# Kernel tuning notes

Hardware: AMD Instinct MI355X
Metric: run time of the kernel (lower is better)

The kernel has to match this reference:

```python
import jax, jax.numpy as jnp
import numpy as np

TEMP = 0.7
TOPK_RATIO = 0.75
BN_EPS = 1e-5  # eval-mode BN with running_mean=0, running_var=1


def conv3x3(x, w):
    # x: [N,C,H,W], w: [O,I,3,3], stride 1, pad 1
    return jax.lax.conv_general_dilated(x, w, (1, 1), 'SAME',
                                        dimension_numbers=('NCHW', 'OIHW', 'NCHW'))


def bn(x, g, b):
    scale = g / jnp.sqrt(1.0 + BN_EPS)
    return x * scale[:, None, None] + b[:, None, None]


def glu(x):
    c = x.shape[1] // 2
    return x[:, :c] * jax.nn.sigmoid(x[:, c:])


def resblock(x, w1, g1, b1, w2, g2, b2):
    out = glu(bn(conv3x3(x, w1), g1, b1))
    out = bn(conv3x3(out, w2), g2, b2)
    return out + x


def refined_attention(h_code, word_embs, w_ctx, mask):
    B, C, H, W = h_code.shape
    Q = H * W
    S = word_embs.shape[2]
    # conv_context is a 1x1 conv (no bias): pure channel projection
    sourceT = jnp.einsum('oc,bcs->bos', w_ctx, word_embs)   # [B, idf, S]
    target = h_code.reshape(B, C, Q)                        # [B, idf, Q]
    attn = jnp.einsum('bcq,bcs->bqs', target, sourceT)      # [B, Q, S]
    attn = attn.reshape(B * Q, S) / TEMP
    # faithful to torch: mask.repeat(queryL, 1) tiles mask over rows
    mask_exp = jnp.tile(mask, (Q, 1))                       # [B*Q, S]
    attn = jnp.where(mask_exp, -jnp.inf, attn)
    if TOPK_RATIO < 1.0 and S > 1:
        k = max(1, int(S * TOPK_RATIO))
        topk_vals, _ = jax.lax.top_k(attn, k)               # sorted desc
        threshold = topk_vals[:, -1:]                       # min of top-k
        attn = jnp.where(attn < threshold, -jnp.inf, attn)
    p = jax.nn.softmax(attn, axis=1)
    nan_rows = jnp.any(jnp.isnan(p), axis=1, keepdims=True)
    p = jnp.where(nan_rows, 1.0 / S, p)                     # uniform fallback
    p = p.reshape(B, Q, S)
    attn_t = jnp.swapaxes(p, 1, 2)                          # [B, S, Q]
    wctx = jnp.einsum('bos,bsq->boq', sourceT, attn_t).reshape(B, C, H, W)
    att_map = attn_t.reshape(B, S, H, W)
    return wctx, att_map


def upsample2x(x):
    return jnp.repeat(jnp.repeat(x, 2, axis=2), 2, axis=3)


def reference(h_code, c_code, word_embs, w_ctx,
              r0_w1, r0_g1, r0_b1, r0_w2, r0_g2, r0_b2,
              r1_w1, r1_g1, r1_b1, r1_w2, r1_g2, r1_b2,
              up_w, up_g, up_b, mask):
    # c_code is in the signature of NEXT_STAGE_G.forward but unused (as in AttnGAN)
    c_code_att, att = refined_attention(h_code, word_embs, w_ctx, mask)
    h_c = jnp.concatenate([h_code, c_code_att], axis=1)     # [B, 2*ngf, H, W]
    out = resblock(h_c, r0_w1, r0_g1, r0_b1, r0_w2, r0_g2, r0_b2)
    out = resblock(out, r1_w1, r1_g1, r1_b1, r1_w2, r1_g2, r1_b2)
    # upBlock: nearest upsample x2 -> conv3x3(2ngf, 2ngf) -> BN -> GLU -> ngf
    out = glu(bn(conv3x3(upsample2x(out), up_w), up_g, up_b))
    return out, att


def setup_inputs() -> dict:
    key = jax.random.key(0)
    ks = jax.random.split(key, 24)
    B, ngf, H, W = 8, 64, 128, 128
    nef, ncf, S = 256, 100, 32
    C2 = 2 * ngf  # 128
    std = 0.02
    inp = {
        'h_code': jax.random.normal(ks[0], (B, ngf, H, W), jnp.float32),
        'c_code': jax.random.normal(ks[1], (B, ncf), jnp.float32),
        'word_embs': jax.random.normal(ks[2], (B, nef, S), jnp.float32),
        'mask': jax.random.randint(ks[3], (B, S), 0, 2).astype(bool),
        'w_ctx': jax.random.normal(ks[4], (ngf, nef), jnp.float32) * std,
    }
    for i, base in enumerate([5, 11]):
        inp[f'r{i}_w1'] = jax.random.normal(ks[base + 0], (2 * C2, C2, 3, 3), jnp.float32) * std
        inp[f'r{i}_g1'] = jnp.ones((2 * C2,), jnp.float32)
        inp[f'r{i}_b1'] = jnp.zeros((2 * C2,), jnp.float32)
        inp[f'r{i}_w2'] = jax.random.normal(ks[base + 3], (C2, C2, 3, 3), jnp.float32) * std
        inp[f'r{i}_g2'] = jnp.ones((C2,), jnp.float32)
        inp[f'r{i}_b2'] = jnp.zeros((C2,), jnp.float32)
    inp['up_w'] = jax.random.normal(ks[17], (2 * ngf, C2, 3, 3), jnp.float32) * std
    inp['up_g'] = jnp.ones((2 * ngf,), jnp.float32)
    inp['up_b'] = jnp.zeros((2 * ngf,), jnp.float32)
    return inp
```

## Files before the change

### kernel.cpp

```cpp
#include <hip/hip_runtime.h>
#include <math.h>


#define B_N 8
#define NGF 64
#define HC 128
#define WC 128
#define QN (HC*WC)
#define NEF 256
#define SN 32
#define TEMP_INV (1.0f/0.7f)
#define BN_SC 0.99999500003749969f
#define TOPK 24

typedef _Float16 f16;
typedef __attribute__((ext_vector_type(8))) _Float16 f16x8;
typedef __attribute__((ext_vector_type(4))) _Float16 f16x4;
typedef __attribute__((ext_vector_type(4))) float f32x4;

__device__ __forceinline__ void gload16(const void* g, void* l) {
    __builtin_amdgcn_global_load_lds(
        (const __attribute__((address_space(1))) void*)g,
        (__attribute__((address_space(3))) void*)l,
        16, 0, 0);
}

__global__ void prep_mask_k(const void* __restrict__ mraw,
                            unsigned* __restrict__ mbits,
                            unsigned* __restrict__ zp) {
    __shared__ int mode;
    if (threadIdx.x == 0) {
        const unsigned* u = (const unsigned*)mraw;
        bool i32 = true, f32m = true;
        for (int i = 0; i < 64; ++i) {
            unsigned v = u[i];
            if (v > 1u) i32 = false;
            if (v != 0u && v != 0x3F800000u) f32m = false;
        }
        mode = i32 ? 0 : (f32m ? 1 : 2);
    }
    __syncthreads();
    int t = threadIdx.x;
    if (t < 64) zp[(t >> 4) * 262144 + (t & 15)] = 0u;
    if (t < B_N) {
        unsigned bits = 0;
        for (int s = 0; s < SN; ++s) {
            int idx = t * SN + s;
            bool on;
            if (mode == 0)      on = ((const int*)mraw)[idx] != 0;
            else if (mode == 1) on = ((const float*)mraw)[idx] != 0.0f;
            else                on = ((const unsigned char*)mraw)[idx] != 0;
            if (on) bits |= (1u << s);
        }
        mbits[t] = bits;
    }
}

__global__ __launch_bounds__(256) void source_t_k(
        const float* __restrict__ w_ctx, const float* __restrict__ word_embs,
        float* __restrict__ sT) {
    int b = blockIdx.x >> 3;
    int o = ((blockIdx.x & 7) << 3) + (threadIdx.x >> 5);
    int s = threadIdx.x & 31;
    const float* wrow = w_ctx + (size_t)o * NEF;
    const float* wb = word_embs + (size_t)b * NEF * SN + s;
    float acc = 0.0f;
    #pragma unroll 8
    for (int c = 0; c < NEF; ++c) acc += wrow[c] * wb[(size_t)c * SN];
    sT[((size_t)b * NGF + o) * SN + s] = acc;
}

__global__ __launch_bounds__(256) void attention_k(
        const float* __restrict__ h_code, const float* __restrict__ sT,
        const unsigned* __restrict__ mbits,
        float* __restrict__ att_out,
        f16* __restrict__ hc) {
    int r0 = blockIdx.x * 256;
    int b = r0 >> 14;
    __shared__ float st[NGF * SN];
    const float* stg = sT + (size_t)b * NGF * SN;
    for (int i = threadIdx.x; i < NGF * SN; i += 256) st[i] = stg[i];
    __syncthreads();
    int q = (r0 & (QN - 1)) + threadIdx.x;

    const float* hb = h_code + (size_t)b * NGF * QN + q;
    f16* hcb = hc + (size_t)b * QN * 128;

    float a[SN];
    #pragma unroll
    for (int s = 0; s < SN; ++s) a[s] = 0.0f;
    for (int g8 = 0; g8 < 8; ++g8) {
        f16x8 t;
        #pragma unroll
        for (int r = 0; r < 8; ++r) {
            float v = hb[(size_t)(g8 * 8 + r) * QN];
            t[r] = (f16)v;
            #pragma unroll
            for (int s = 0; s < SN; ++s) a[s] += v * st[(g8 * 8 + r) * SN + s];
        }
        *(f16x8*)(hcb + ((size_t)g8 * QN + q) * 8) = t;
    }
    unsigned mb = mbits[q & 7];
    #pragma unroll
    for (int s = 0; s < SN; ++s)
        a[s] = ((mb >> s) & 1u) ? -INFINITY : a[s] * TEMP_INV;

    float thr = -INFINITY;
    #pragma unroll
    for (int s = 0; s < SN; ++s) {
        int rank = 0;
        #pragma unroll
        for (int j = 0; j < SN; ++j)
            rank += (a[j] > a[s]) || (a[j] == a[s] && j < s);
        if (rank == TOPK - 1) thr = a[s];
    }
    float m = -INFINITY;
    #pragma unroll
    for (int s = 0; s < SN; ++s) {
        if (a[s] < thr) a[s] = -INFINITY;
        m = fmaxf(m, a[s]);
    }
    float p[SN];
    if (m == -INFINITY) {
        #pragma unroll
        for (int s = 0; s < SN; ++s) p[s] = 1.0f / SN;
    } else {
        float sum = 0.0f;
        #pragma unroll
        for (int s = 0; s < SN; ++s) { p[s] = __expf(a[s] - m); sum += p[s]; }
        float inv = 1.0f / sum;
        #pragma unroll
        for (int s = 0; s < SN; ++s) p[s] *= inv;
    }
    float* ao = att_out + (size_t)b * SN * QN + q;
    #pragma unroll
    for (int s = 0; s < SN; ++s) ao[(size_t)s * QN] = p[s];
    for (int g8 = 0; g8 < 8; ++g8) {
        f16x8 t;
        #pragma unroll
        for (int r = 0; r < 8; ++r) {
            float acc = 0.0f;
            #pragma unroll
            for (int s = 0; s < SN; ++s) acc += st[(g8 * 8 + r) * SN + s] * p[s];
            t[r] = (f16)acc;
        }
        *(f16x8*)(hcb + ((size_t)(8 + g8) * QN + q) * 8) = t;
    }
}

__global__ __launch_bounds__(256) void wt_transform_k(
        const float* __restrict__ w, f16* __restrict__ wt,
        int total, int HALF ) {
    int idx = blockIdx.x * 256 + threadIdx.x;
    if (idx >= total) return;
    int e   = idx & 7;
    int gp  = (idx >> 3) & 3;
    int cop = (idx >> 5) & 63;
    int u   = idx >> 11;
    int t   = u % 9;
    int v   = u / 9;
    int cc  = v & 3;
    int cb  = v >> 2;
    int g   = gp ^ ((cop >> 1) & 3);
    int ci  = cc * 32 + g * 8 + e;
    int co  = HALF ? (cop < 32 ? cb * 32 + cop : HALF + cb * 32 + (cop - 32))
                   : cb * 64 + cop;
    wt[idx] = (f16)w[((size_t)co * 128 + ci) * 9 + t];
}

__global__ __launch_bounds__(256) void wt_up_transform_k(
        const float* __restrict__ w, f16* __restrict__ wt) {
    int idx = blockIdx.x * 256 + threadIdx.x;
    int e   = idx & 7;
    int gp  = (idx >> 3) & 3;
    int cop = (idx >> 5) & 63;
    int tap = (idx >> 11) & 3;
    int pw  = (idx >> 13) & 1;
    int cc  = (idx >> 14) & 3;
    int ph  = (idx >> 16) & 1;
    int cb  = (idx >> 17) & 1;
    int g   = gp ^ ((cop >> 1) & 3);
    int ci  = cc * 32 + g * 8 + e;
    int co  = cop < 32 ? cb * 32 + cop : 64 + cb * 32 + (cop - 32);
    int ra = tap >> 1, bb = tap & 1;
    const float* wp = w + ((size_t)co * 128 + ci) * 9;
    float acc = 0.0f;
    #pragma unroll
    for (int kh = 0; kh < 3; ++kh) {
        int rma = (ph == 0) ? (kh == 0 ? 0 : 1) : (kh == 2 ? 1 : 0);
        if (rma != ra) continue;
        #pragma unroll
        for (int kw = 0; kw < 3; ++kw) {
            int cma = (pw == 0) ? (kw == 0 ? 0 : 1) : (kw == 2 ? 1 : 0);
            if (cma == bb) acc += wp[kh * 3 + kw];
        }
    }
    wt[idx] = (f16)acc;
}

template<int COUT, bool GLU, bool RES, bool UP, int HOUT, int WOUT, bool FINAL>
__global__ __launch_bounds__(256) void conv_mfma_k(
        const f16* __restrict__ in, const f16* __restrict__ wt,
        const float* __restrict__ gamma, const float* __restrict__ beta,
        const f16* __restrict__ res, f16* __restrict__ outh,
        float* __restrict__ outf, const char* __restrict__ zeros) {
    constexpr int HALF = COUT / 2;
    constexpr int OCH  = GLU ? HALF : COUT;
    constexpr int HIN  = UP ? HOUT / 2 : HOUT;
    constexpr int WIN  = UP ? WOUT / 2 : WOUT;
    constexpr int RPT  = 256 / WOUT;
    constexpr int ROWS_IN = UP ? 2 : RPT + 2;
    constexpr int NIN_G   = ROWS_IN * 520;
    constexpr int NIN_IT  = (NIN_G + 255) / 256;
    constexpr int NIN_PAD = NIN_IT * 256;
    constexpr int NTAP    = UP ? 4 : 9;
    constexpr int WBYTES  = UP ? 32768 : 36864;
    constexpr int WIT     = WBYTES / 4096;

    __shared__ char smem[NIN_PAD * 16 + WBYTES];
    char* sW = smem + NIN_PAD * 16;

    const int tid = threadIdx.x, lane = tid & 63, wv = tid >> 6;
    const int l15 = lane & 15, kg = lane >> 4;
    const int b = blockIdx.z, cb = blockIdx.y, qt = blockIdx.x;
    const int q0 = qt * 256;
    const int h0 = q0 / WOUT;
    const int ph = UP ? (h0 & 1) : 0;
    const int p  = wv >> 1;
    const int jq = ((wv & 1) << 6) + l15;

    f32x4 acc[4][4];
    #pragma unroll
    for (int m = 0; m < 4; ++m)
        #pragma unroll
        for (int n = 0; n < 4; ++n) acc[m][n] = (f32x4){0.f, 0.f, 0.f, 0.f};

    const f16* inb = in + (size_t)b * HIN * WIN * 128;
    const char* wtb = UP
        ? (const char*)wt + (size_t)(cb * 2 + ph) * 131072
        : (const char*)wt + (size_t)cb * 147456;

    const char* srcK[NIN_IT];
    #pragma unroll
    for (int k = 0; k < NIN_IT; ++k) {
        int idx = (k << 8) + tid;
        int r = idx / 520;
        int rem = idx - r * 520;
        int wi = rem >> 2, gp = rem & 3;
        int g = gp ^ ((wi >> 1) & 3);
        const char* s = zeros;
        if (UP) {
            int sh = (h0 >> 1) + r - 1 + ph;
            int sw = wi - 1;
            if (r < 2 && (unsigned)sh < (unsigned)HIN && (unsigned)sw < (unsigned)WIN)
                s = (const char*)(inb + (((size_t)g * (HIN * WIN) + (size_t)sh * WIN + sw) << 3));
        } else {
            int gh = h0 - 1 + r;
            int gw = wi - 1;
            if (r < ROWS_IN && (unsigned)gh < (unsigned)HOUT && (unsigned)gw < (unsigned)WOUT)
                s = (const char*)(inb + (((size_t)g * (HIN * WIN) + (size_t)gh * WIN + gw) << 3));
        }
        srcK[k] = s;
    }
    const int dstB = (tid & 192) << 4;

    for (int cc = 0; cc < 4; ++cc) {
        #pragma unroll
        for (int k = 0; k < NIN_IT; ++k)
            gload16(srcK[k] + (cc << 20), smem + (k << 12) + dstB);
        const char* wsrc = wtb + cc * WBYTES + (tid << 4);
        #pragma unroll
        for (int k = 0; k < WIT; ++k)
            gload16(wsrc + (k << 12), sW + (k << 12) + dstB);
        __syncthreads();

        #pragma unroll
        for (int t = 0; t < NTAP; ++t) {
            f16x8 af[4], bf[4];
            const int tapbase = UP ? ((p * 4 + t) << 12) : (t << 12);
            #pragma unroll
            for (int m = 0; m < 4; ++m) {
                int co = m * 16 + l15;
                af[m] = *(const f16x8*)(sW + tapbase + (co << 6)
                                        + ((kg ^ ((co >> 1) & 3)) << 4));
            }
            #pragma unroll
            for (int n = 0; n < 4; ++n) {
                int off;
                if (UP) {
                    int si = jq + (n << 4) + (t & 1) + p;
                    off = (t >> 1) * 8320 + si * 64 + ((kg ^ ((si >> 1) & 3)) << 4);
                } else {
                    const int kh = t / 3, kw = t % 3;
                    int row = (wv >> 1) + kh;
                    int wi = ((wv & 1) << 6) + (n << 4) + l15 + kw;
                    off = row * 8320 + wi * 64 + ((kg ^ ((wi >> 1) & 3)) << 4);
                }
                bf[n] = *(const f16x8*)(smem + off);
            }
            #pragma unroll
            for (int m = 0; m < 4; ++m)
                #pragma unroll
                for (int n = 0; n < 4; ++n)
                    acc[m][n] = __builtin_amdgcn_mfma_f32_16x16x32_f16(af[m], bf[n], acc[m][n], 0, 0, 0);
        }
        __syncthreads();
    }

    const int r4 = kg * 4;
    if (GLU) {
        #pragma unroll
        for (int mv = 0; mv < 2; ++mv) {
            const int v0 = cb * 32 + mv * 16 + r4;
            float s1[4], o1[4], s2[4], o2[4];
            #pragma unroll
            for (int r = 0; r < 4; ++r) {
                s1[r] = gamma[v0 + r] * BN_SC;        o1[r] = beta[v0 + r];
                s2[r] = gamma[v0 + r + HALF] * BN_SC; o2[r] = beta[v0 + r + HALF];
            }
            #pragma unroll
            for (int n = 0; n < 4; ++n) {
                float ov[4];
                #pragma unroll
                for (int r = 0; r < 4; ++r) {
                    float yv = acc[mv][n][r] * s1[r] + o1[r];
                    float zv = acc[mv + 2][n][r] * s2[r] + o2[r];
                    ov[r] = yv / (1.0f + __expf(-zv));
                }
                if (FINAL) {
                    const int w = UP ? 2 * (jq + (n << 4)) + p
                                     : ((wv << 6) + (n << 4) + l15) % WOUT;
                    const int h = UP ? h0 : h0 + ((wv << 6) + (n << 4) + l15) / WOUT;
                    #pragma unroll
                    for (int r = 0; r < 4; ++r)
                        outf[(((size_t)b * OCH + v0 + r) * HOUT + h) * WOUT + w] = ov[r];
                } else {
                    const int qc = (wv << 6) + (n << 4) + l15;
                    f16x4 tv;
                    #pragma unroll
                    for (int r = 0; r < 4; ++r) tv[r] = (f16)ov[r];
                    *(f16x4*)(outh + ((((size_t)b * (OCH / 8) + (v0 >> 3)) << 14)
                                      + q0 + qc) * 8 + (v0 & 7)) = tv;
                }
            }
        }
    } else {
        #pragma unroll
        for (int m = 0; m < 4; ++m) {
            const int c0 = cb * 64 + m * 16 + r4;
            float s[4], o[4];
            #pragma unroll
            for (int r = 0; r < 4; ++r) {
                s[r] = gamma[c0 + r] * BN_SC; o[r] = beta[c0 + r];
            }
            #pragma unroll
            for (int n = 0; n < 4; ++n) {
                const int qc = (wv << 6) + (n << 4) + l15;
                const size_t gaddr = ((((size_t)b * 16 + (c0 >> 3)) << 14) + q0 + qc) * 8 + (c0 & 7);
                float ov[4];
                #pragma unroll
                for (int r = 0; r < 4; ++r) ov[r] = acc[m][n][r] * s[r] + o[r];
                if (RES) {
                    f16x4 rv = *(const f16x4*)(res + gaddr);
                    #pragma unroll
                    for (int r = 0; r < 4; ++r) ov[r] += (float)rv[r];
                }
                f16x4 tv;
                #pragma unroll
                for (int r = 0; r < 4; ++r) tv[r] = (f16)ov[r];
                *(f16x4*)(outh + gaddr) = tv;
            }
        }
    }
}

extern "C" void kernel_launch(void* const* d_in, const int* in_sizes, int n_in,
                              void* d_out, int out_size, void* d_ws, size_t ws_size,
                              hipStream_t stream) {
    (void)in_sizes; (void)n_in; (void)out_size; (void)ws_size;
    const float* h_code    = (const float*)d_in[0];
    const float* word_embs = (const float*)d_in[2];
    const void*  mask      = d_in[3];
    const float* w_ctx     = (const float*)d_in[4];
    const float* r0_w1 = (const float*)d_in[5];
    const float* r0_g1 = (const float*)d_in[6];
    const float* r0_b1 = (const float*)d_in[7];
    const float* r0_w2 = (const float*)d_in[8];
    const float* r0_g2 = (const float*)d_in[9];
    const float* r0_b2 = (const float*)d_in[10];
    const float* r1_w1 = (const float*)d_in[11];
    const float* r1_g1 = (const float*)d_in[12];
    const float* r1_b1 = (const float*)d_in[13];
    const float* r1_w2 = (const float*)d_in[14];
    const float* r1_g2 = (const float*)d_in[15];
    const float* r1_b2 = (const float*)d_in[16];
    const float* up_w  = (const float*)d_in[17];
    const float* up_g  = (const float*)d_in[18];
    const float* up_b  = (const float*)d_in[19];

    float* outp = (float*)d_out;
    float* attp = outp + (size_t)B_N * NGF * 4 * HC * WC;

    unsigned* mbits = (unsigned*)d_ws;
    float* sT  = (float*)((char*)d_ws + 1024);
    char* zeros = (char*)d_ws + ((size_t)4 << 20);
    f16* hcA   = (f16*)((char*)d_ws + ((size_t)8 << 20));
    f16* wtbuf = (f16*)((char*)d_ws + ((size_t)40 << 20));

    const int W1_TOT = 4 * 4 * 9 * 64 * 32;
    const int W2_TOT = 2 * 4 * 9 * 64 * 32;
    const int WUP_TOT = 2 * 2 * 4 * 2 * 4 * 64 * 32;
    f16* Wr0c1 = wtbuf;
    f16* Wr0c2 = Wr0c1 + W1_TOT;
    f16* Wr1c1 = Wr0c2 + W2_TOT;
    f16* Wr1c2 = Wr1c1 + W1_TOT;
    f16* Wup   = Wr1c2 + W2_TOT;

    f16* Bbuf = (f16*)d_out;
    f16* Cbuf = (f16*)((char*)d_out + ((size_t)32 << 20));

    prep_mask_k<<<1, 64, 0, stream>>>(mask, mbits, (unsigned*)zeros);
    source_t_k<<<64, 256, 0, stream>>>(w_ctx, word_embs, sT);

    wt_transform_k<<<(W1_TOT + 255) / 256, 256, 0, stream>>>(r0_w1, Wr0c1, W1_TOT, 128);
    wt_transform_k<<<(W2_TOT + 255) / 256, 256, 0, stream>>>(r0_w2, Wr0c2, W2_TOT, 0);
    wt_transform_k<<<(W1_TOT + 255) / 256, 256, 0, stream>>>(r1_w1, Wr1c1, W1_TOT, 128);
    wt_transform_k<<<(W2_TOT + 255) / 256, 256, 0, stream>>>(r1_w2, Wr1c2, W2_TOT, 0);
    wt_up_transform_k<<<WUP_TOT / 256, 256, 0, stream>>>(up_w, Wup);

    attention_k<<<(B_N * QN) / 256, 256, 0, stream>>>(h_code, sT, mbits, attp, hcA);

    conv_mfma_k<256, true,  false, false, 128, 128, false>
        <<<dim3(64, 4, B_N), 256, 0, stream>>>(hcA, Wr0c1, r0_g1, r0_b1, nullptr, Bbuf, nullptr, zeros);
    conv_mfma_k<128, false, true,  false, 128, 128, false>
        <<<dim3(64, 2, B_N), 256, 0, stream>>>(Bbuf, Wr0c2, r0_g2, r0_b2, hcA, Cbuf, nullptr, zeros);
    conv_mfma_k<256, true,  false, false, 128, 128, false>
        <<<dim3(64, 4, B_N), 256, 0, stream>>>(Cbuf, Wr1c1, r1_g1, r1_b1, nullptr, Bbuf, nullptr, zeros);
    conv_mfma_k<128, false, true,  false, 128, 128, false>
        <<<dim3(64, 2, B_N), 256, 0, stream>>>(Bbuf, Wr1c2, r1_g2, r1_b2, Cbuf, hcA, nullptr, zeros);
    conv_mfma_k<128, true,  false, true,  256, 256, true>
        <<<dim3(256, 2, B_N), 256, 0, stream>>>(hcA, Wup, up_g, up_b, nullptr, nullptr, outp, zeros);
}
```

Baseline: 404.3 us.

## Split upsample conv into dedicated 512-thread kernel sharing input rows across row pairs

Moves the upsample+conv+GLU stage out of the generic conv template into its own kernel. Each 512-thread block covers two output rows of the same phase, which read three overlapping input rows, so the staged input and the per-phase weights are reused across twice the output. This halves the block count and cuts redundant global-to-LDS traffic for input and weights. The cost is a larger block and more LDS per block, which may lower occupancy.

```diff
diff --git a/kernel.cpp b/kernel.cpp
--- a/kernel.cpp
+++ b/kernel.cpp
@@ -198,24 +198,23 @@
     wt[idx] = (f16)acc;
 }
 
-template<int COUT, bool GLU, bool RES, bool UP, int HOUT, int WOUT, bool FINAL>
+template<int COUT, bool GLU, bool RES, int HOUT, int WOUT>
 __global__ __launch_bounds__(256) void conv_mfma_k(
         const f16* __restrict__ in, const f16* __restrict__ wt,
         const float* __restrict__ gamma, const float* __restrict__ beta,
         const f16* __restrict__ res, f16* __restrict__ outh,
-        float* __restrict__ outf, const char* __restrict__ zeros) {
+        const char* __restrict__ zeros) {
     constexpr int HALF = COUT / 2;
     constexpr int OCH  = GLU ? HALF : COUT;
-    constexpr int HIN  = UP ? HOUT / 2 : HOUT;
-    constexpr int WIN  = UP ? WOUT / 2 : WOUT;
+    constexpr int HIN  = HOUT;
+    constexpr int WIN  = WOUT;
     constexpr int RPT  = 256 / WOUT;
-    constexpr int ROWS_IN = UP ? 2 : RPT + 2;
+    constexpr int ROWS_IN = RPT + 2;
     constexpr int NIN_G   = ROWS_IN * 520;
     constexpr int NIN_IT  = (NIN_G + 255) / 256;
     constexpr int NIN_PAD = NIN_IT * 256;
-    constexpr int NTAP    = UP ? 4 : 9;
-    constexpr int WBYTES  = UP ? 32768 : 36864;
-    constexpr int WIT     = WBYTES / 4096;
+    constexpr int WBYTES  = 36864;
+    constexpr int WIT     = 9;
 
     __shared__ char smem[NIN_PAD * 16 + WBYTES];
     char* sW = smem + NIN_PAD * 16;
@@ -225,9 +224,6 @@
     const int b = blockIdx.z, cb = blockIdx.y, qt = blockIdx.x;
     const int q0 = qt * 256;
     const int h0 = q0 / WOUT;
-    const int ph = UP ? (h0 & 1) : 0;
-    const int p  = wv >> 1;
-    const int jq = ((wv & 1) << 6) + l15;
 
     f32x4 acc[4][4];
     #pragma unroll
@@ -236,9 +232,7 @@
         for (int n = 0; n < 4; ++n) acc[m][n] = (f32x4){0.f, 0.f, 0.f, 0.f};
 
     const f16* inb = in + (size_t)b * HIN * WIN * 128;
-    const char* wtb = UP
-        ? (const char*)wt + (size_t)(cb * 2 + ph) * 131072
-        : (const char*)wt + (size_t)cb * 147456;
+    const char* wtb = (const char*)wt + (size_t)cb * 147456;
 
     const char* srcK[NIN_IT];
     #pragma unroll
@@ -248,18 +242,11 @@
         int rem = idx - r * 520;
         int wi = rem >> 2, gp = rem & 3;
         int g = gp ^ ((wi >> 1) & 3);
+        int gh = h0 - 1 + r;
+        int gw = wi - 1;
         const char* s = zeros;
-        if (UP) {
-            int sh = (h0 >> 1) + r - 1 + ph;
-            int sw = wi - 1;
-            if (r < 2 && (unsigned)sh < (unsigned)HIN && (unsigned)sw < (unsigned)WIN)
-                s = (const char*)(inb + (((size_t)g * (HIN * WIN) + (size_t)sh * WIN + sw) << 3));
-        } else {
-            int gh = h0 - 1 + r;
-            int gw = wi - 1;
-            if (r < ROWS_IN && (unsigned)gh < (unsigned)HOUT && (unsigned)gw < (unsigned)WOUT)
-                s = (const char*)(inb + (((size_t)g * (HIN * WIN) + (size_t)gh * WIN + gw) << 3));
-        }
+        if (r < ROWS_IN && (unsigned)gh < (unsigned)HOUT && (unsigned)gw < (unsigned)WOUT)
+            s = (const char*)(inb + (((size_t)g * (HIN * WIN) + (size_t)gh * WIN + gw) << 3));
         srcK[k] = s;
     }
     const int dstB = (tid & 192) << 4;
@@ -275,27 +262,20 @@
         __syncthreads();
 
         #pragma unroll
-        for (int t = 0; t < NTAP; ++t) {
+        for (int t = 0; t < 9; ++t) {
             f16x8 af[4], bf[4];
-            const int tapbase = UP ? ((p * 4 + t) << 12) : (t << 12);
             #pragma unroll
             for (int m = 0; m < 4; ++m) {
                 int co = m * 16 + l15;
-                af[m] = *(const f16x8*)(sW + tapbase + (co << 6)
+                af[m] = *(const f16x8*)(sW + (t << 12) + (co << 6)
                                         + ((kg ^ ((co >> 1) & 3)) << 4));
             }
             #pragma unroll
             for (int n = 0; n < 4; ++n) {
-                int off;
-                if (UP) {
-                    int si = jq + (n << 4) + (t & 1) + p;
-                    off = (t >> 1) * 8320 + si * 64 + ((kg ^ ((si >> 1) & 3)) << 4);
-                } else {
-                    const int kh = t / 3, kw = t % 3;
-                    int row = (wv >> 1) + kh;
-                    int wi = ((wv & 1) << 6) + (n << 4) + l15 + kw;
-                    off = row * 8320 + wi * 64 + ((kg ^ ((wi >> 1) & 3)) << 4);
-                }
+                const int kh = t / 3, kw = t % 3;
+                int row = (wv >> 1) + kh;
+                int wi = ((wv & 1) << 6) + (n << 4) + l15 + kw;
+                int off = row * 8320 + wi * 64 + ((kg ^ ((wi >> 1) & 3)) << 4);
                 bf[n] = *(const f16x8*)(smem + off);
             }
             #pragma unroll
@@ -327,21 +307,12 @@
                     float zv = acc[mv + 2][n][r] * s2[r] + o2[r];
                     ov[r] = yv / (1.0f + __expf(-zv));
                 }
-                if (FINAL) {
-                    const int w = UP ? 2 * (jq + (n << 4)) + p
-                                     : ((wv << 6) + (n << 4) + l15) % WOUT;
-                    const int h = UP ? h0 : h0 + ((wv << 6) + (n << 4) + l15) / WOUT;
-                    #pragma unroll
-                    for (int r = 0; r < 4; ++r)
-                        outf[(((size_t)b * OCH + v0 + r) * HOUT + h) * WOUT + w] = ov[r];
-                } else {
-                    const int qc = (wv << 6) + (n << 4) + l15;
-                    f16x4 tv;
-                    #pragma unroll
-                    for (int r = 0; r < 4; ++r) tv[r] = (f16)ov[r];
-                    *(f16x4*)(outh + ((((size_t)b * (OCH / 8) + (v0 >> 3)) << 14)
-                                      + q0 + qc) * 8 + (v0 & 7)) = tv;
-                }
+                const int qc = (wv << 6) + (n << 4) + l15;
+                f16x4 tv;
+                #pragma unroll
+                for (int r = 0; r < 4; ++r) tv[r] = (f16)ov[r];
+                *(f16x4*)(outh + ((((size_t)b * (OCH / 8) + (v0 >> 3)) << 14)
+                                  + q0 + qc) * 8 + (v0 & 7)) = tv;
             }
         }
     } else {
@@ -370,6 +341,114 @@
                 for (int r = 0; r < 4; ++r) tv[r] = (f16)ov[r];
                 *(f16x4*)(outh + gaddr) = tv;
             }
+        }
+    }
+}
+
+__global__ __launch_bounds__(512) void conv_up_k(
+        const f16* __restrict__ in, const f16* __restrict__ wt,
+        const float* __restrict__ gamma, const float* __restrict__ beta,
+        float* __restrict__ outf, const char* __restrict__ zeros) {
+    constexpr int HIN = 128, WIN = 128;
+    __shared__ char smem[24960 + 32768];
+    char* sW = smem + 24960;
+
+    const int tid = threadIdx.x, lane = tid & 63, wv = tid >> 6;
+    const int l15 = lane & 15, kg = lane >> 4;
+    const int b = blockIdx.z, cb = blockIdx.y;
+    const int j = blockIdx.x >> 1, ph = blockIdx.x & 1;
+    const int rr = wv >> 2;
+    const int p  = (wv >> 1) & 1;
+    const int jq = ((wv & 1) << 6) + l15;
+
+    f32x4 acc[4][4];
+    #pragma unroll
+    for (int m = 0; m < 4; ++m)
+        #pragma unroll
+        for (int n = 0; n < 4; ++n) acc[m][n] = (f32x4){0.f, 0.f, 0.f, 0.f};
+
+    const f16* inb = in + (size_t)b * HIN * WIN * 128;
+    const char* wtb = (const char*)wt + (size_t)(cb * 2 + ph) * 131072;
+
+    const char* srcK[4];
+    #pragma unroll
+    for (int k = 0; k < 4; ++k) {
+        int idx = (k < 3) ? ((k << 9) + tid) : (1536 + tid);
+        int r = idx / 520;
+        int rem = idx - r * 520;
+        int wi = rem >> 2, gp = rem & 3;
+        int g = gp ^ ((wi >> 1) & 3);
+        int sh = 2 * j - 1 + ph + r;
+        int sw = wi - 1;
+        const char* s = zeros;
+        if (r < 3 && (unsigned)sh < (unsigned)HIN && (unsigned)sw < (unsigned)WIN)
+            s = (const char*)(inb + (((size_t)g * (HIN * WIN) + (size_t)sh * WIN + sw) << 3));
+        srcK[k] = s;
+    }
+    const int dstB = (tid & 448) << 4;
+
+    for (int cc = 0; cc < 4; ++cc) {
+        #pragma unroll
+        for (int k = 0; k < 3; ++k)
+            gload16(srcK[k] + (cc << 20), smem + (k << 13) + dstB);
+        if (tid < 24)
+            gload16(srcK[3] + (cc << 20), smem + 24576);
+        const char* wsrc = wtb + cc * 32768 + (tid << 4);
+        #pragma unroll
+        for (int k = 0; k < 4; ++k)
+            gload16(wsrc + (k << 13), sW + (k << 13) + dstB);
+        __syncthreads();
+
+        #pragma unroll
+        for (int t = 0; t < 4; ++t) {
+            f16x8 af[4], bf[4];
+            const int tapbase = (p * 4 + t) << 12;
+            #pragma unroll
+            for (int m = 0; m < 4; ++m) {
+                int co = m * 16 + l15;
+                af[m] = *(const f16x8*)(sW + tapbase + (co << 6)
+                                        + ((kg ^ ((co >> 1) & 3)) << 4));
+            }
+            #pragma unroll
+            for (int n = 0; n < 4; ++n) {
+                int si = jq + (n << 4) + (t & 1) + p;
+                int off = (rr + (t >> 1)) * 8320 + si * 64
+                          + ((kg ^ ((si >> 1) & 3)) << 4);
+                bf[n] = *(const f16x8*)(smem + off);
+            }
+            #pragma unroll
+            for (int m = 0; m < 4; ++m)
+                #pragma unroll
+                for (int n = 0; n < 4; ++n)
+                    acc[m][n] = __builtin_amdgcn_mfma_f32_16x16x32_f16(af[m], bf[n], acc[m][n], 0, 0, 0);
+        }
+        __syncthreads();
+    }
+
+    const int r4 = kg * 4;
+    const int h = 4 * j + 2 * rr + ph;
+    #pragma unroll
+    for (int mv = 0; mv < 2; ++mv) {
+        const int v0 = cb * 32 + mv * 16 + r4;
+        float s1[4], o1[4], s2[4], o2[4];
+        #pragma unroll
+        for (int r = 0; r < 4; ++r) {
+            s1[r] = gamma[v0 + r] * BN_SC;      o1[r] = beta[v0 + r];
+            s2[r] = gamma[v0 + r + 64] * BN_SC; o2[r] = beta[v0 + r + 64];
+        }
+        #pragma unroll
+        for (int n = 0; n < 4; ++n) {
+            const int w = 2 * (jq + (n << 4)) + p;
+            float ov[4];
+            #pragma unroll
+            for (int r = 0; r < 4; ++r) {
+                float yv = acc[mv][n][r] * s1[r] + o1[r];
+                float zv = acc[mv + 2][n][r] * s2[r] + o2[r];
+                ov[r] = yv / (1.0f + __expf(-zv));
+            }
+            #pragma unroll
+            for (int r = 0; r < 4; ++r)
+                outf[(((size_t)b * 64 + v0 + r) * 256 + h) * 256 + w] = ov[r];
         }
     }
 }
@@ -430,14 +509,13 @@
 
     attention_k<<<(B_N * QN) / 256, 256, 0, stream>>>(h_code, sT, mbits, attp, hcA);
 
-    conv_mfma_k<256, true,  false, false, 128, 128, false>
-        <<<dim3(64, 4, B_N), 256, 0, stream>>>(hcA, Wr0c1, r0_g1, r0_b1, nullptr, Bbuf, nullptr, zeros);
-    conv_mfma_k<128, false, true,  false, 128, 128, false>
-        <<<dim3(64, 2, B_N), 256, 0, stream>>>(Bbuf, Wr0c2, r0_g2, r0_b2, hcA, Cbuf, nullptr, zeros);
-    conv_mfma_k<256, true,  false, false, 128, 128, false>
-        <<<dim3(64, 4, B_N), 256, 0, stream>>>(Cbuf, Wr1c1, r1_g1, r1_b1, nullptr, Bbuf, nullptr, zeros);
-    conv_mfma_k<128, false, true,  false, 128, 128, false>
-        <<<dim3(64, 2, B_N), 256, 0, stream>>>(Bbuf, Wr1c2, r1_g2, r1_b2, Cbuf, hcA, nullptr, zeros);
-    conv_mfma_k<128, true,  false, true,  256, 256, true>
-        <<<dim3(256, 2, B_N), 256, 0, stream>>>(hcA, Wup, up_g, up_b, nullptr, nullptr, outp, zeros);
-}
+    conv_mfma_k<256, true,  false, 128, 128>
+        <<<dim3(64, 4, B_N), 256, 0, stream>>>(hcA, Wr0c1, r0_g1, r0_b1, nullptr, Bbuf, zeros);
+    conv_mfma_k<128, false, true,  128, 128>
+        <<<dim3(64, 2, B_N), 256, 0, stream>>>(Bbuf, Wr0c2, r0_g2, r0_b2, hcA, Cbuf, zeros);
+    conv_mfma_k<256, true,  false, 128, 128>
+        <<<dim3(64, 4, B_N), 256, 0, stream>>>(Cbuf, Wr1c1, r1_g1, r1_b1, nullptr, Bbuf, zeros);
+    conv_mfma_k<128, false, true,  128, 128>
+        <<<dim3(64, 2, B_N), 256, 0, stream>>>(Bbuf, Wr1c2, r1_g2, r1_b2, Cbuf, hcA, zeros);
+    conv_up_k<<<dim3(128, 2, B_N), 512, 0, stream>>>(hcA, Wup, up_g, up_b, outp, zeros);
+}
```

New measurement: 401.9 us. No clear change (-0.6%).
